# Optimization experiments

Hardware: AMD Instinct MI355X
Metric: run time of the kernel (lower is better)

## Reference

```python
import jax, jax.numpy as jnp
import numpy as np

D_MODEL = 1024
NUM_HEADS = 16
D_K = D_MODEL // NUM_HEADS
FFN_SIZE = 4096
EPS = 1e-6


def _layer_norm(x, gamma, beta):
    mu = jnp.mean(x, axis=-1, keepdims=True)
    var = jnp.var(x, axis=-1, keepdims=True)
    return (x - mu) / jnp.sqrt(var + EPS) * gamma + beta


def setup_inputs() -> dict:
    key = jax.random.key(0)
    ks = jax.random.split(key, 12)
    B, S = 2, 2048
    s_attn = 1.0 / np.sqrt(D_MODEL)
    s_ffn1 = 1.0 / np.sqrt(D_MODEL)
    s_ffn2 = 1.0 / np.sqrt(FFN_SIZE)
    return {
        "x": jax.random.normal(ks[0], (B, S, D_MODEL), dtype=jnp.float32),
        "W_q": jax.random.normal(ks[1], (D_MODEL, D_MODEL), dtype=jnp.float32) * s_attn,
        "W_k": jax.random.normal(ks[2], (D_MODEL, D_MODEL), dtype=jnp.float32) * s_attn,
        "W_v": jax.random.normal(ks[3], (D_MODEL, D_MODEL), dtype=jnp.float32) * s_attn,
        "W_o": jax.random.normal(ks[4], (D_MODEL, D_MODEL), dtype=jnp.float32) * s_attn,
        "b_o": jnp.zeros((D_MODEL,), dtype=jnp.float32),
        "W1": jax.random.normal(ks[5], (D_MODEL, FFN_SIZE), dtype=jnp.float32) * s_ffn1,
        "b1": jnp.zeros((FFN_SIZE,), dtype=jnp.float32),
        "W2": jax.random.normal(ks[6], (FFN_SIZE, D_MODEL), dtype=jnp.float32) * s_ffn2,
        "b2": jnp.zeros((D_MODEL,), dtype=jnp.float32),
        "ln1_g": jnp.ones((D_MODEL,), dtype=jnp.float32),
        "ln1_b": jnp.zeros((D_MODEL,), dtype=jnp.float32),
        "ln2_g": jnp.ones((D_MODEL,), dtype=jnp.float32),
        "ln2_b": jnp.zeros((D_MODEL,), dtype=jnp.float32),
    }


def reference(x, W_q, W_k, W_v, W_o, b_o, W1, b1, W2, b2,
              ln1_g, ln1_b, ln2_g, ln2_b):
    B, S, _ = x.shape

    # --- self-attention sublayer (pre-norm residual) ---
    h = _layer_norm(x, ln1_g, ln1_b)
    q = (h @ W_q).reshape(B, S, NUM_HEADS, D_K).transpose(0, 2, 1, 3)  # [B,H,S,Dk]
    k = (h @ W_k).reshape(B, S, NUM_HEADS, D_K).transpose(0, 2, 1, 3)
    v = (h @ W_v).reshape(B, S, NUM_HEADS, D_K).transpose(0, 2, 1, 3)
    scores = jnp.einsum("bhqd,bhkd->bhqk", q, k) / jnp.sqrt(jnp.float32(D_K))
    attn = jax.nn.softmax(scores, axis=-1)
    ctx = jnp.einsum("bhqk,bhkd->bhqd", attn, v)
    ctx = ctx.transpose(0, 2, 1, 3).reshape(B, S, D_MODEL)
    x = x + (ctx @ W_o + b_o)

    # --- FFN sublayer (pre-norm residual) ---
    h2 = _layer_norm(x, ln2_g, ln2_b)
    f = jax.nn.relu(h2 @ W1 + b1) @ W2 + b2
    return x + f
```

## Files before the change

kernel.cpp:

```cpp
#include <hip/hip_runtime.h>
#include <cstdint>
#include <cstddef>


typedef __attribute__((ext_vector_type(8))) __bf16 bf16x8;
typedef __attribute__((ext_vector_type(4))) __bf16 bf16x4;
typedef __attribute__((ext_vector_type(4))) float f32x4;

__device__ __forceinline__ void async16(const void* g, void* l) {
  __builtin_amdgcn_global_load_lds(
      (__attribute__((address_space(1))) void*)g,
      (__attribute__((address_space(3))) void*)l, 16, 0, 0);
}

__device__ __forceinline__ f32x4 mfma16(bf16x8 a, bf16x8 b, f32x4 c) {
  return __builtin_amdgcn_mfma_f32_16x16x32_bf16(a, b, c, 0, 0, 0);
}

template <int N>
__device__ __forceinline__ void wait_vmcnt() {
  if constexpr (N == 0) {
    asm volatile("s_waitcnt vmcnt(0)" ::: "memory");
  } else if constexpr (N == 3) {
    asm volatile("s_waitcnt vmcnt(3)" ::: "memory");
  } else {
    asm volatile("s_waitcnt vmcnt(4)" ::: "memory");
  }
}
__device__ __forceinline__ void barrier_raw() {
  asm volatile("s_barrier" ::: "memory");
}
__device__ __forceinline__ void lgkm0() {
  asm volatile("s_waitcnt lgkmcnt(0)" ::: "memory");
}

__global__ __launch_bounds__(256) void transpose_all(
    const float* __restrict__ Wq, const float* __restrict__ Wk,
    const float* __restrict__ Wv, const float* __restrict__ Wo,
    const float* __restrict__ W1, const float* __restrict__ W2,
    __bf16* __restrict__ WqkvT, __bf16* __restrict__ WoT,
    __bf16* __restrict__ W1T, __bf16* __restrict__ W2T) {
  const int id = blockIdx.x;
  const float* in;
  __bf16* out;
  int ld_in, ld_out, c0, r0;
  if (id < 1024) {
    const int which = id >> 8, tl = id & 255;
    c0 = (tl & 15) * 64;
    r0 = (tl >> 4) * 64;
    ld_in = 1024;
    ld_out = 1024;
    if (which == 0) { in = Wq; out = WqkvT; }
    else if (which == 1) { in = Wk; out = WqkvT + 1048576; }
    else if (which == 2) { in = Wv; out = WqkvT + 2097152; }
    else { in = Wo; out = WoT; }
  } else if (id < 2048) {
    const int tl = id - 1024;
    c0 = (tl & 63) * 64;
    r0 = (tl >> 6) * 64;
    in = W1; out = W1T; ld_in = 4096; ld_out = 1024;
  } else {
    const int tl = id - 2048;
    c0 = (tl & 15) * 64;
    r0 = (tl >> 4) * 64;
    in = W2; out = W2T; ld_in = 1024; ld_out = 4096;
  }
  __shared__ __bf16 tile[64][65];
  const int tx = threadIdx.x & 63, ty = threadIdx.x >> 6;
#pragma unroll
  for (int i = 0; i < 16; i++) {
    int r = ty + i * 4;
    tile[r][tx] = (__bf16)in[(size_t)(r0 + r) * ld_in + c0 + tx];
  }
  __syncthreads();
#pragma unroll
  for (int i = 0; i < 16; i++) {
    int r = ty + i * 4;
    out[(size_t)(c0 + r) * ld_out + r0 + tx] = tile[tx][r];
  }
}

__global__ __launch_bounds__(256) void transpose_bf16(
    const unsigned short* __restrict__ in, unsigned short* __restrict__ out,
    int ld_in, int ld_out) {
  __shared__ unsigned short tile[64][65];
  const int c0 = blockIdx.x * 64, r0 = blockIdx.y * 64;
  const int tx = threadIdx.x & 63, ty = threadIdx.x >> 6;
#pragma unroll
  for (int i = 0; i < 16; i++) {
    int r = ty + i * 4;
    tile[r][tx] = in[(size_t)(r0 + r) * ld_in + c0 + tx];
  }
  __syncthreads();
#pragma unroll
  for (int i = 0; i < 16; i++) {
    int r = ty + i * 4;
    out[(size_t)(c0 + r) * ld_out + r0 + tx] = tile[tx][r];
  }
}

__global__ __launch_bounds__(256) void ln_kernel(
    const float* __restrict__ xin, const float* __restrict__ g,
    const float* __restrict__ bt, __bf16* __restrict__ out) {
  const int tok = blockIdx.x * 4 + (threadIdx.x >> 6);
  const int lane = threadIdx.x & 63;
  const int base0 = lane * 8, base1 = 512 + lane * 8;
  const float* xr = xin + (size_t)tok * 1024;
  float v[16];
  float4 a0 = *(const float4*)(xr + base0);
  float4 a1 = *(const float4*)(xr + base0 + 4);
  float4 a2 = *(const float4*)(xr + base1);
  float4 a3 = *(const float4*)(xr + base1 + 4);
  v[0] = a0.x; v[1] = a0.y; v[2] = a0.z; v[3] = a0.w;
  v[4] = a1.x; v[5] = a1.y; v[6] = a1.z; v[7] = a1.w;
  v[8] = a2.x; v[9] = a2.y; v[10] = a2.z; v[11] = a2.w;
  v[12] = a3.x; v[13] = a3.y; v[14] = a3.z; v[15] = a3.w;
  float s = 0.f, s2 = 0.f;
#pragma unroll
  for (int i = 0; i < 16; i++) { s += v[i]; s2 += v[i] * v[i]; }
#pragma unroll
  for (int m = 1; m < 64; m <<= 1) {
    s += __shfl_xor(s, m);
    s2 += __shfl_xor(s2, m);
  }
  const float mean = s * (1.f / 1024.f);
  const float var = s2 * (1.f / 1024.f) - mean * mean;
  const float rstd = rsqrtf(var + 1e-6f);
  float4 g0 = *(const float4*)(g + base0), g1 = *(const float4*)(g + base0 + 4);
  float4 g2 = *(const float4*)(g + base1), g3 = *(const float4*)(g + base1 + 4);
  float4 b0 = *(const float4*)(bt + base0), b1v = *(const float4*)(bt + base0 + 4);
  float4 b2v = *(const float4*)(bt + base1), b3 = *(const float4*)(bt + base1 + 4);
  float gg[16] = {g0.x, g0.y, g0.z, g0.w, g1.x, g1.y, g1.z, g1.w,
                  g2.x, g2.y, g2.z, g2.w, g3.x, g3.y, g3.z, g3.w};
  float bb[16] = {b0.x, b0.y, b0.z, b0.w, b1v.x, b1v.y, b1v.z, b1v.w,
                  b2v.x, b2v.y, b2v.z, b2v.w, b3.x, b3.y, b3.z, b3.w};
  bf16x8 o0, o1;
#pragma unroll
  for (int j = 0; j < 8; j++) {
    o0[j] = (__bf16)((v[j] - mean) * rstd * gg[j] + bb[j]);
    o1[j] = (__bf16)((v[8 + j] - mean) * rstd * gg[8 + j] + bb[8 + j]);
  }
  __bf16* op = out + (size_t)tok * 1024;
  *(bf16x8*)(op + base0) = o0;
  *(bf16x8*)(op + base1) = o1;
}

template <int EPI, int SPLITS = 1>
__global__ __launch_bounds__(512, 2) void gemm256(
    const __bf16* __restrict__ A, int lda, const __bf16* __restrict__ BT,
    int ldb, void* __restrict__ C, int ldc, int Kb,
    const float* __restrict__ bias) {
  const int t = threadIdx.x;
  const int m0 = blockIdx.x * 256, n0 = blockIdx.y * 256;
  const int kz = (SPLITS > 1) ? blockIdx.z : 0;
  __shared__ __align__(16) __bf16 As[2][2][8192];
  __shared__ __align__(16) __bf16 Bs[2][2][8192];
  const int lane = t & 63;
  const int quad = lane >> 4, l15 = lane & 15;
  const int w = t >> 6, wm = w >> 2, wn = w & 3;

  f32x4 acc[8][4] = {};

  const int rr = t >> 3;
  const int ca = (t & 7) ^ (rr & 7);
  const int cc = rr & 31;
  const int wnb = t >> 8;
  const int cb = (t & 7) ^ (cc & 7);
  const __bf16* gA = A + (size_t)kz * Kb + (size_t)(m0 + rr) * lda + ca * 8;
  const __bf16* gB = BT + (size_t)kz * Kb +
                     (size_t)(n0 + wnb * 64 + cc) * ldb + cb * 8;
  const size_t a64 = (size_t)64 * lda, a128 = (size_t)128 * lda;
  const size_t b32 = (size_t)32 * ldb, b128 = (size_t)128 * ldb;

  auto stageA = [&](int buf, int mq, int ko) {
    const __bf16* g = gA + (mq ? a64 : 0) + ko;
    __bf16* l = &As[buf][mq][t * 8];
    async16(g, l);
    async16(g + a128, l + 4096);
  };
  auto stageB = [&](int buf, int nq, int ko) {
    const __bf16* g = gB + (nq ? b32 : 0) + ko;
    __bf16* l = &Bs[buf][nq][t * 8];
    async16(g, l);
    async16(g + b128, l + 4096);
  };

  const int arow = wm * 4096 + l15 * 64;
  const int brow = wn * 2048 + l15 * 64;
  const int x7 = l15 & 7;

  auto loadA = [&](int buf, int mq, bf16x8 (&af)[4][2]) {
#pragma unroll
    for (int mi = 0; mi < 4; mi++)
#pragma unroll
      for (int kk = 0; kk < 2; kk++)
        af[mi][kk] = *(const bf16x8*)&As[buf][mq]
            [arow + mi * 1024 + (((kk * 4 + quad) ^ x7) * 8)];
  };
  auto loadB = [&](int buf, int nq, bf16x8 (&bv)[2][2]) {
#pragma unroll
    for (int ni = 0; ni < 2; ni++)
#pragma unroll
      for (int kk = 0; kk < 2; kk++)
        bv[ni][kk] = *(const bf16x8*)&Bs[buf][nq]
            [brow + ni * 1024 + (((kk * 4 + quad) ^ x7) * 8)];
  };
  auto mm = [&](int mq, int nq, const bf16x8 (&af)[4][2],
                const bf16x8 (&bv)[2][2]) {
    __builtin_amdgcn_s_setprio(1);
#pragma unroll
    for (int mi = 0; mi < 4; mi++)
#pragma unroll
      for (int ni = 0; ni < 2; ni++)
#pragma unroll
        for (int kk = 0; kk < 2; kk++)
          acc[mq * 4 + mi][nq * 2 + ni] =
              mfma16(af[mi][kk], bv[ni][kk], acc[mq * 4 + mi][nq * 2 + ni]);
    __builtin_amdgcn_s_setprio(0);
  };

  const int NT = Kb / 64;
  stageA(0, 0, 0); stageB(0, 0, 0); stageA(0, 1, 0); stageB(0, 1, 0);
  stageA(1, 0, 64); stageB(1, 0, 64);
  wait_vmcnt<4>();
  barrier_raw();

  bf16x8 af[4][2], b0[2][2], b1[2][2];
  for (int s = 0; s < NT; ++s) {
    const int buf = s & 1;
    const int ko1 = (s + 1) * 64, ko2 = (s + 2) * 64;
    loadA(buf, 0, af);
    loadB(buf, 0, b0);
    if (s + 1 < NT) stageA(buf ^ 1, 1, ko1);
    barrier_raw();
    lgkm0();
    mm(0, 0, af, b0);
    barrier_raw();
    loadB(buf, 1, b1);
    if (s + 1 < NT) stageB(buf ^ 1, 1, ko1);
    barrier_raw();
    lgkm0();
    mm(0, 1, af, b1);
    barrier_raw();
    loadA(buf, 1, af);
    if (s + 2 < NT) stageA(buf, 0, ko2);
    barrier_raw();
    lgkm0();
    mm(1, 0, af, b0);
    barrier_raw();
    if (s + 2 < NT) {
      stageB(buf, 0, ko2);
      wait_vmcnt<4>();
    } else {
      wait_vmcnt<0>();
    }
    barrier_raw();
    mm(1, 1, af, b1);
    barrier_raw();
  }

  float biasv[4];
  if constexpr (EPI == 2) {
#pragma unroll
    for (int ni = 0; ni < 4; ni++)
      biasv[ni] = bias[n0 + wn * 64 + ni * 16 + l15];
  }
  __bf16* Cb = (__bf16*)C;
  if constexpr (SPLITS > 1)
    Cb += (size_t)kz * (size_t)gridDim.x * 256 * ldc;
#pragma unroll
  for (int mi = 0; mi < 8; mi++)
#pragma unroll
    for (int ni = 0; ni < 4; ni++)
#pragma unroll
      for (int r = 0; r < 4; r++) {
        const int row = m0 + wm * 128 + mi * 16 + quad * 4 + r;
        const int col = n0 + wn * 64 + ni * 16 + l15;
        float v = acc[mi][ni][r];
        if constexpr (EPI == 0) {
          Cb[(size_t)row * ldc + col] = (__bf16)v;
        } else {
          v += biasv[ni];
          Cb[(size_t)row * ldc + col] = (__bf16)fmaxf(v, 0.f);
        }
      }
}

template <int EPI, int TM, int SPLITS = 1>
__global__ __launch_bounds__(256) void gemm_bt(
    const __bf16* __restrict__ A, int lda, const __bf16* __restrict__ BT,
    int ldb, void* __restrict__ C, int ldc, int Kb,
    const float* __restrict__ bias, const float* __restrict__ res, int ldres) {
  const int t = threadIdx.x;
  const int m0 = blockIdx.x * TM, n0 = blockIdx.y * 128;
  const int kz = (SPLITS > 1) ? blockIdx.z : 0;
  __shared__ __align__(16) __bf16 As[3][TM * 32];
  __shared__ __align__(16) __bf16 Bs[3][128 * 32];
  const int lane = t & 63, w = t >> 6;
  const int quad = lane >> 4, l15 = lane & 15;
  const int wm = w >> 1, wn = w & 1;
  constexpr int MF = TM / 32;
  constexpr int LOADS = TM / 64 + 2;

  f32x4 acc[MF][4] = {};

  const int swc = ((t & 3) ^ ((t >> 3) & 3)) * 8;
  const __bf16* ga = A + (size_t)(m0 + (t >> 2)) * lda + swc + (size_t)kz * Kb;
  const __bf16* gb = BT + (size_t)(n0 + (t >> 2)) * ldb + swc + (size_t)kz * Kb;
  const size_t a64 = (size_t)64 * lda, b64 = (size_t)64 * ldb;

  auto stage = [&](int buf) {
#pragma unroll
    for (int i = 0; i < TM / 64; i++)
      async16(ga + i * a64, As[buf] + t * 8 + i * 2048);
    async16(gb, Bs[buf] + t * 8);
    async16(gb + b64, Bs[buf] + t * 8 + 2048);
    ga += 32;
    gb += 32;
  };
  const int ce = (quad ^ ((l15 >> 1) & 3)) * 8;
  auto compute = [&](int buf) {
    bf16x8 af[MF], bfr[4];
#pragma unroll
    for (int i = 0; i < MF; i++)
      af[i] = *(const bf16x8*)&As[buf][(wm * (TM / 2) + i * 16 + l15) * 32 + ce];
#pragma unroll
    for (int i = 0; i < 4; i++)
      bfr[i] = *(const bf16x8*)&Bs[buf][(wn * 64 + i * 16 + l15) * 32 + ce];
#pragma unroll
    for (int mi = 0; mi < MF; mi++)
#pragma unroll
      for (int ni = 0; ni < 4; ni++)
        acc[mi][ni] = mfma16(af[mi], bfr[ni], acc[mi][ni]);
  };

  const int iters = Kb / 32;
  stage(0);
  stage(1);
  int cur = 0, stg = 2;
  for (int it = 0; it < iters - 1; ++it) {
    wait_vmcnt<LOADS>();
    barrier_raw();
    if (it + 2 < iters) stage(stg);
    compute(cur);
    cur = (cur == 2) ? 0 : cur + 1;
    stg = (stg == 2) ? 0 : stg + 1;
  }
  wait_vmcnt<0>();
  barrier_raw();
  compute(cur);

  float biasv[4];
  if constexpr (EPI != 0) {
#pragma unroll
    for (int ni = 0; ni < 4; ni++)
      biasv[ni] = bias[n0 + wn * 64 + ni * 16 + l15];
  }
  __bf16* Cb = (__bf16*)C;
  if constexpr (SPLITS > 1)
    Cb += (size_t)kz * gridDim.x * TM * ldc;
#pragma unroll
  for (int mi = 0; mi < MF; mi++)
#pragma unroll
    for (int ni = 0; ni < 4; ni++)
#pragma unroll
      for (int r = 0; r < 4; r++) {
        const int row = m0 + wm * (TM / 2) + mi * 16 + quad * 4 + r;
        const int col = n0 + wn * 64 + ni * 16 + l15;
        float v = acc[mi][ni][r];
        if constexpr (EPI == 0) {
          Cb[(size_t)row * ldc + col] = (__bf16)v;
        } else if constexpr (EPI == 1) {
          v += biasv[ni] + res[(size_t)row * ldres + col];
          ((float*)C)[(size_t)row * ldc + col] = v;
        } else {
          v += biasv[ni];
          ((__bf16*)C)[(size_t)row * ldc + col] = (__bf16)fmaxf(v, 0.f);
        }
      }
}

__global__ __launch_bounds__(256) void reduce_split4(
    const __bf16* __restrict__ P, const float* __restrict__ bias,
    const float* __restrict__ res, float* __restrict__ out) {
  const int row = blockIdx.x, c = threadIdx.x * 4;
  const size_t i = (size_t)row * 1024 + c;
  float4 r = *(const float4*)(res + i);
  float4 bv = *(const float4*)(bias + c);
  float s0 = r.x + bv.x, s1 = r.y + bv.y, s2 = r.z + bv.z, s3 = r.w + bv.w;
#pragma unroll
  for (int j = 0; j < 4; j++) {
    bf16x4 p = *(const bf16x4*)(P + (size_t)j * 4194304 + i);
    s0 += (float)p[0];
    s1 += (float)p[1];
    s2 += (float)p[2];
    s3 += (float)p[3];
  }
  float4 o = {s0, s1, s2, s3};
  *(float4*)(out + i) = o;
}

__global__ __launch_bounds__(256, 2) void attn_kernel(
    const __bf16* __restrict__ QKV, const __bf16* __restrict__ VT,
    __bf16* __restrict__ ctx) {
  const int qt = blockIdx.x, bh = blockIdx.y;
  const int b = bh >> 4, h = bh & 15;
  const int t = threadIdx.x, w = t >> 6, lane = t & 63;
  const int quad = lane >> 4, l15 = lane & 15;
  const int tok0 = b * 2048;
  const int q0w = tok0 + qt * 128 + w * 32;

  __shared__ __align__(16) __bf16 Ks[2][128 * 64];
  __shared__ __align__(16) __bf16 VTs[2][64 * 128];

  const float qs = 0.18033688011112042f;
  bf16x8 qf[2][2];
#pragma unroll
  for (int mi = 0; mi < 2; mi++)
#pragma unroll
    for (int kb = 0; kb < 2; kb++) {
      const __bf16* src = QKV + (size_t)(q0w + mi * 16 + l15) * 3072 + h * 64 +
                          kb * 32 + quad * 8;
      bf16x8 r = *(const bf16x8*)src;
#pragma unroll
      for (int j = 0; j < 8; j++) r[j] = (__bf16)((float)r[j] * qs);
      qf[mi][kb] = r;
    }

  f32x4 lacc[2] = {};
  f32x4 O[2][4] = {};

  const int krow = t >> 3;
  const int kcg = (((t & 7) ^ (krow & 7)) * 8);
  const int vrow = t >> 4;
  const int vcg = (((2 * (t & 15)) ^ ((vrow & 7) * 2)) * 4);
  const int sub = 4 * (quad & 1);
  const int qh = quad >> 1;

  auto stage = [&](int buf, int kt) {
    const int ktok = tok0 + kt * 128;
#pragma unroll
    for (int j = 0; j < 4; j++) {
      const __bf16* gp =
          QKV + (size_t)(ktok + krow + j * 32) * 3072 + 1024 + h * 64 + kcg;
      async16(gp, Ks[buf] + t * 8 + j * 2048);
    }
#pragma unroll
    for (int j = 0; j < 4; j++) {
      const __bf16* gp =
          VT + (size_t)(h * 64 + vrow + j * 16) * 4096 + ktok + vcg;
      async16(gp, VTs[buf] + t * 8 + j * 2048);
    }
  };

  stage(0, 0);
  wait_vmcnt<0>();
  barrier_raw();

  int buf = 0;
  for (int kt = 0; kt < 16; ++kt) {
    if (kt + 1 < 16) stage(buf ^ 1, kt + 1);

    f32x4 sT[2][8];
#pragma unroll
    for (int kt8 = 0; kt8 < 8; kt8++) {
      f32x4 a0 = {}, a1 = {};
#pragma unroll
      for (int kb = 0; kb < 2; kb++) {
        bf16x8 kf = *(const bf16x8*)&Ks[buf][(kt8 * 16 + l15) * 64 +
                                            (((kb * 4 + quad) ^ (l15 & 7)) * 8)];
        a0 = mfma16(kf, qf[0][kb], a0);
        a1 = mfma16(kf, qf[1][kb], a1);
      }
      sT[0][kt8] = a0;
      sT[1][kt8] = a1;
    }

    bf16x8 pf[2][4];
#pragma unroll
    for (int mi = 0; mi < 2; mi++)
#pragma unroll
      for (int kb = 0; kb < 4; kb++)
#pragma unroll
        for (int hf = 0; hf < 2; hf++)
#pragma unroll
          for (int r = 0; r < 4; r++) {
            const float p = __builtin_amdgcn_exp2f(sT[mi][2 * kb + hf][r]);
            lacc[mi][r] += p;
            pf[mi][kb][hf * 4 + r] = (__bf16)p;
          }

#pragma unroll
    for (int kb = 0; kb < 4; kb++) {
      const int g0 = (((4 * kb + qh) ^ (l15 & 7)) * 8) + sub;
      const int g1 = (((4 * kb + 2 + qh) ^ (l15 & 7)) * 8) + sub;
#pragma unroll
      for (int nd = 0; nd < 4; nd++) {
        const int base = (nd * 16 + l15) * 128;
        bf16x4 a0 = *(const bf16x4*)&VTs[buf][base + g0];
        bf16x4 a1 = *(const bf16x4*)&VTs[buf][base + g1];
        bf16x8 vf;
        vf[0] = a0[0]; vf[1] = a0[1]; vf[2] = a0[2]; vf[3] = a0[3];
        vf[4] = a1[0]; vf[5] = a1[1]; vf[6] = a1[2]; vf[7] = a1[3];
        O[0][nd] = mfma16(pf[0][kb], vf, O[0][nd]);
        O[1][nd] = mfma16(pf[1][kb], vf, O[1][nd]);
      }
    }

    wait_vmcnt<0>();
    barrier_raw();
    buf ^= 1;
  }

#pragma unroll
  for (int mi = 0; mi < 2; mi++) {
    float lsum = lacc[mi][0] + lacc[mi][1] + lacc[mi][2] + lacc[mi][3];
    lsum += __shfl_xor(lsum, 16);
    lsum += __shfl_xor(lsum, 32);
    float rl[4];
#pragma unroll
    for (int r = 0; r < 4; r++) rl[r] = 1.0f / __shfl(lsum, quad * 4 + r);
#pragma unroll
    for (int nd = 0; nd < 4; nd++)
#pragma unroll
      for (int r = 0; r < 4; r++) {
        const int tokq = q0w + mi * 16 + quad * 4 + r;
        const int col = h * 64 + nd * 16 + l15;
        ctx[(size_t)tokq * 1024 + col] = (__bf16)(O[mi][nd][r] * rl[r]);
      }
  }
}

extern "C" void kernel_launch(void* const* d_in, const int* in_sizes, int n_in,
                              void* d_out, int out_size, void* d_ws,
                              size_t ws_size, hipStream_t stream) {
  (void)in_sizes; (void)n_in; (void)out_size; (void)ws_size;

  const float* x = (const float*)d_in[0];
  const float* Wq = (const float*)d_in[1];
  const float* Wk = (const float*)d_in[2];
  const float* Wv = (const float*)d_in[3];
  const float* Wo = (const float*)d_in[4];
  const float* b_o = (const float*)d_in[5];
  const float* W1 = (const float*)d_in[6];
  const float* b1 = (const float*)d_in[7];
  const float* W2 = (const float*)d_in[8];
  const float* b2 = (const float*)d_in[9];
  const float* ln1g = (const float*)d_in[10];
  const float* ln1b = (const float*)d_in[11];
  const float* ln2g = (const float*)d_in[12];
  const float* ln2b = (const float*)d_in[13];

  char* ws = (char*)d_ws;
  __bf16* h = (__bf16*)(ws + 0);
  __bf16* W1T = (__bf16*)(ws + 8388608);
  __bf16* WqkvT = (__bf16*)(ws + 16777216);
  __bf16* WoT = (__bf16*)(ws + 23068672);
  __bf16* QKV = (__bf16*)(ws + 25165824);
  __bf16* VT = (__bf16*)(ws + 50331648);
  __bf16* ctx = (__bf16*)(ws + 58720256);
  __bf16* f1 = (__bf16*)(ws + 33554432);
  __bf16* Pw2 = (__bf16*)(ws + 0);
  float* x1 = (float*)(ws + 67108864);
  __bf16* W2T = (__bf16*)(ws + 83886080);

  const dim3 blk(256);
  const dim3 blk512(512);

  transpose_all<<<dim3(3072), blk, 0, stream>>>(Wq, Wk, Wv, Wo, W1, W2, WqkvT,
                                                WoT, W1T, W2T);

  ln_kernel<<<dim3(1024), blk, 0, stream>>>(x, ln1g, ln1b, h);

  gemm256<0><<<dim3(16, 12), blk512, 0, stream>>>(
      h, 1024, WqkvT, 1024, (void*)QKV, 3072, 1024, nullptr);

  transpose_bf16<<<dim3(16, 64), blk, 0, stream>>>(
      (const unsigned short*)(QKV + 2048), (unsigned short*)VT, 3072, 4096);

  attn_kernel<<<dim3(16, 32), blk, 0, stream>>>(QKV, VT, ctx);

  gemm_bt<1, 64><<<dim3(64, 8), blk, 0, stream>>>(
      ctx, 1024, WoT, 1024, (void*)x1, 1024, 1024, b_o, x, 1024);

  ln_kernel<<<dim3(1024), blk, 0, stream>>>(x1, ln2g, ln2b, h);

  gemm256<2><<<dim3(16, 16), blk512, 0, stream>>>(
      h, 1024, W1T, 1024, (void*)f1, 4096, 1024, b1);

  gemm256<0, 4><<<dim3(16, 4, 4), blk512, 0, stream>>>(
      f1, 4096, W2T, 4096, (void*)Pw2, 1024, 1024, nullptr);
  reduce_split4<<<dim3(4096), blk, 0, stream>>>(Pw2, b2, x1, (float*)d_out);
}
```

Measured before the change: 320.5 us.

## Permute V-transpose layout so attention loads one 16B V fragment per MFMA

The V transpose kernel now writes tokens in a permuted order within each 32-token group, so each lane's P·V MFMA operand becomes one contiguous bf16x8 LDS load instead of two bf16x4 loads plus register shuffles. The P fragments are built in the matching interleaved order. The exp/softmax conversion is interleaved per kb block with the P·V MFMAs rather than done all at once, which cuts live registers. s_setprio hints are added around the MFMA sections. Correctness depends on the permutation, the swizzle and the pf element order all agreeing.

```diff
diff --git a/kernel.cpp b/kernel.cpp
--- a/kernel.cpp
+++ b/kernel.cpp
@@ -80,7 +80,7 @@
   }
 }
 
-__global__ __launch_bounds__(256) void transpose_bf16(
+__global__ __launch_bounds__(256) void transpose_vt_perm(
     const unsigned short* __restrict__ in, unsigned short* __restrict__ out,
     int ld_in, int ld_out) {
   __shared__ unsigned short tile[64][65];
@@ -92,10 +92,11 @@
     tile[r][tx] = in[(size_t)(r0 + r) * ld_in + c0 + tx];
   }
   __syncthreads();
+  const int ptx = (tx & 32) + 2 * (tx & 15) + ((tx >> 4) & 1);
 #pragma unroll
   for (int i = 0; i < 16; i++) {
     int r = ty + i * 4;
-    out[(size_t)(c0 + r) * ld_out + r0 + tx] = tile[tx][r];
+    out[(size_t)(c0 + r) * ld_out + r0 + ptx] = tile[tx][r];
   }
 }
 
@@ -434,8 +435,7 @@
   const int kcg = (((t & 7) ^ (krow & 7)) * 8);
   const int vrow = t >> 4;
   const int vcg = (((2 * (t & 15)) ^ ((vrow & 7) * 2)) * 4);
-  const int sub = 4 * (quad & 1);
-  const int qh = quad >> 1;
+  const int x7 = l15 & 7;
 
   auto stage = [&](int buf, int kt) {
     const int ktok = tok0 + kt * 128;
@@ -462,49 +462,45 @@
     if (kt + 1 < 16) stage(buf ^ 1, kt + 1);
 
     f32x4 sT[2][8];
+    __builtin_amdgcn_s_setprio(1);
 #pragma unroll
     for (int kt8 = 0; kt8 < 8; kt8++) {
       f32x4 a0 = {}, a1 = {};
 #pragma unroll
       for (int kb = 0; kb < 2; kb++) {
         bf16x8 kf = *(const bf16x8*)&Ks[buf][(kt8 * 16 + l15) * 64 +
-                                            (((kb * 4 + quad) ^ (l15 & 7)) * 8)];
+                                            (((kb * 4 + quad) ^ x7) * 8)];
         a0 = mfma16(kf, qf[0][kb], a0);
         a1 = mfma16(kf, qf[1][kb], a1);
       }
       sT[0][kt8] = a0;
       sT[1][kt8] = a1;
     }
-
-    bf16x8 pf[2][4];
-#pragma unroll
-    for (int mi = 0; mi < 2; mi++)
-#pragma unroll
-      for (int kb = 0; kb < 4; kb++)
-#pragma unroll
-        for (int hf = 0; hf < 2; hf++)
-#pragma unroll
-          for (int r = 0; r < 4; r++) {
-            const float p = __builtin_amdgcn_exp2f(sT[mi][2 * kb + hf][r]);
-            lacc[mi][r] += p;
-            pf[mi][kb][hf * 4 + r] = (__bf16)p;
-          }
+    __builtin_amdgcn_s_setprio(0);
 
 #pragma unroll
     for (int kb = 0; kb < 4; kb++) {
-      const int g0 = (((4 * kb + qh) ^ (l15 & 7)) * 8) + sub;
-      const int g1 = (((4 * kb + 2 + qh) ^ (l15 & 7)) * 8) + sub;
+      bf16x8 pf0, pf1;
+#pragma unroll
+      for (int hf = 0; hf < 2; hf++)
+#pragma unroll
+        for (int r = 0; r < 4; r++) {
+          const float p0 = __builtin_amdgcn_exp2f(sT[0][2 * kb + hf][r]);
+          const float p1 = __builtin_amdgcn_exp2f(sT[1][2 * kb + hf][r]);
+          lacc[0][r] += p0;
+          lacc[1][r] += p1;
+          pf0[r * 2 + hf] = (__bf16)p0;
+          pf1[r * 2 + hf] = (__bf16)p1;
+        }
+      __builtin_amdgcn_s_setprio(1);
 #pragma unroll
       for (int nd = 0; nd < 4; nd++) {
-        const int base = (nd * 16 + l15) * 128;
-        bf16x4 a0 = *(const bf16x4*)&VTs[buf][base + g0];
-        bf16x4 a1 = *(const bf16x4*)&VTs[buf][base + g1];
-        bf16x8 vf;
-        vf[0] = a0[0]; vf[1] = a0[1]; vf[2] = a0[2]; vf[3] = a0[3];
-        vf[4] = a1[0]; vf[5] = a1[1]; vf[6] = a1[2]; vf[7] = a1[3];
-        O[0][nd] = mfma16(pf[0][kb], vf, O[0][nd]);
-        O[1][nd] = mfma16(pf[1][kb], vf, O[1][nd]);
+        bf16x8 vf = *(const bf16x8*)&VTs[buf][(nd * 16 + l15) * 128 +
+                                             (((4 * kb + quad) ^ x7) * 8)];
+        O[0][nd] = mfma16(pf0, vf, O[0][nd]);
+        O[1][nd] = mfma16(pf1, vf, O[1][nd]);
       }
+      __builtin_amdgcn_s_setprio(0);
     }
 
     wait_vmcnt<0>();
@@ -575,7 +571,7 @@
   gemm256<0><<<dim3(16, 12), blk512, 0, stream>>>(
       h, 1024, WqkvT, 1024, (void*)QKV, 3072, 1024, nullptr);
 
-  transpose_bf16<<<dim3(16, 64), blk, 0, stream>>>(
+  transpose_vt_perm<<<dim3(16, 64), blk, 0, stream>>>(
       (const unsigned short*)(QKV + 2048), (unsigned short*)VT, 3072, 4096);
 
   attn_kernel<<<dim3(16, 32), blk, 0, stream>>>(QKV, VT, ctx);
```

Result: faster. 313.8 us (-2.1%).
